# Kernel tuning notes

Measured on AMD Instinct MI355X. Metric: run time of the kernel, lower is better.

Reference implementation:

```python
import jax, jax.numpy as jnp
import numpy as np

D_MODEL = 1024
N_HEADS = 16
HEAD_DIM = D_MODEL // N_HEADS
B, T = 4, 2048
EPS = 1e-5


def _layernorm(x, w, b):
    mu = jnp.mean(x, axis=-1, keepdims=True)
    var = jnp.mean(jnp.square(x - mu), axis=-1, keepdims=True)
    return (x - mu) * jax.lax.rsqrt(var + EPS) * w + b


def _heads(x, w, b):
    # x: [B,T,D]; w stored [in,out] so y = x @ w + b (== torch Linear)
    y = x @ w + b
    return y.reshape(B, T, N_HEADS, HEAD_DIM).transpose(0, 2, 1, 3)  # [B,H,T,hd]


def _attention(q, k, v):
    scores = jnp.einsum('bhqd,bhkd->bhqk', q, k) / np.sqrt(HEAD_DIM).astype(np.float32)
    attn = jax.nn.softmax(scores, axis=-1)  # dropout is identity in eval mode
    o = jnp.einsum('bhqk,bhkd->bhqd', attn, v)
    return o.transpose(0, 2, 1, 3).reshape(B, T, D_MODEL)


def setup_inputs() -> dict:
    key = jax.random.key(0)
    ks = jax.random.split(key, 16)
    s = 1.0 / np.sqrt(D_MODEL)
    def lin(k, din, dout):
        kw, kb = jax.random.split(k)
        return (jax.random.uniform(kw, (din, dout), jnp.float32, -s, s),
                jax.random.uniform(kb, (dout,), jnp.float32, -s, s))
    inp = {}
    inp['temporal_tokens'] = jax.random.normal(ks[0], (B, T, D_MODEL), jnp.float32)
    inp['feature_tokens'] = jax.random.normal(ks[1], (B, T, D_MODEL), jnp.float32)
    names = ['qt', 'kf', 'vf', 'qf', 'kt', 'vt', 'ot', 'of']
    for i, n in enumerate(names):
        w, b = lin(ks[2 + i], D_MODEL, D_MODEL)
        inp[n + '_w'], inp[n + '_b'] = w, b
    inp['fus1_w'], inp['fus1_b'] = lin(ks[10], 2 * D_MODEL, D_MODEL)
    inp['fus2_w'], inp['fus2_b'] = lin(ks[11], D_MODEL, D_MODEL)
    for n in ['ln_fus', 'ln_t', 'ln_f']:
        inp[n + '_w'] = jnp.ones((D_MODEL,), jnp.float32)
        inp[n + '_b'] = jnp.zeros((D_MODEL,), jnp.float32)
    return inp


def reference(temporal_tokens, feature_tokens,
              qt_w, qt_b, kf_w, kf_b, vf_w, vf_b,
              qf_w, qf_b, kt_w, kt_b, vt_w, vt_b,
              ot_w, ot_b, of_w, of_b,
              fus1_w, fus1_b, fus2_w, fus2_b,
              ln_fus_w, ln_fus_b, ln_t_w, ln_t_b, ln_f_w, ln_f_b):
    # temporal -> feature cross attention
    Qt = _heads(temporal_tokens, qt_w, qt_b)
    Kf = _heads(feature_tokens, kf_w, kf_b)
    Vf = _heads(feature_tokens, vf_w, vf_b)
    attn_t = _attention(Qt, Kf, Vf) @ ot_w + ot_b
    fused_t = _layernorm(temporal_tokens + attn_t, ln_t_w, ln_t_b)
    # feature -> temporal cross attention
    Qf = _heads(feature_tokens, qf_w, qf_b)
    Kt = _heads(temporal_tokens, kt_w, kt_b)
    Vt = _heads(temporal_tokens, vt_w, vt_b)
    attn_f = _attention(Qf, Kt, Vt) @ of_w + of_b
    fused_f = _layernorm(feature_tokens + attn_f, ln_f_w, ln_f_b)
    # fusion MLP
    combined = jnp.concatenate([fused_t, fused_f], axis=-1)  # [B,T,2D]
    h = jax.nn.gelu(combined @ fus1_w + fus1_b, approximate=False)
    fused = _layernorm(h @ fus2_w + fus2_b, ln_fus_w, ln_fus_b)
    return fused
```

## Files before the change

### kernel.cpp

```cpp
#include <hip/hip_runtime.h>
#include <math.h>

typedef __attribute__((ext_vector_type(8))) short short8;
typedef __attribute__((ext_vector_type(4))) short short4v;
typedef __attribute__((ext_vector_type(4))) float floatx4;

#define GLOBAL_AS __attribute__((address_space(1)))
#define LDS_AS __attribute__((address_space(3)))

__device__ __forceinline__ float bf2f(unsigned short u) {
    unsigned int x = ((unsigned int)u) << 16;
    return __builtin_bit_cast(float, x);
}
__device__ __forceinline__ unsigned short f2bf(float f) {
    unsigned int u = __builtin_bit_cast(unsigned int, f);
    u += 0x7fffu + ((u >> 16) & 1u);
    return (unsigned short)(u >> 16);
}

__global__ __launch_bounds__(256) void cvt2_kernel(
    const float* __restrict__ a, const float* __restrict__ b,
    unsigned short* __restrict__ oa, unsigned short* __restrict__ ob)
{
    const int bx = blockIdx.x;
    const float* in = bx < 8192 ? a : b;
    unsigned short* out = bx < 8192 ? oa : ob;
    const size_t i = ((size_t)(bx & 8191) * 256 + threadIdx.x) * 4;
    float4 f = *(const float4*)(in + i);
    unsigned short o[4] = {f2bf(f.x), f2bf(f.y), f2bf(f.z), f2bf(f.w)};
    *(uint2*)(out + i) = *(const uint2*)o;
}

struct WX {
    const float* src[10];
    unsigned long long dst[10];
    int r64[10];
    int cum[11];
};

__global__ __launch_bounds__(256) void transpose_all_kernel(WX P, unsigned short* __restrict__ base)
{
    __shared__ unsigned short T[64][72];
    const int bx = blockIdx.x;
    int w = 0;
    #pragma unroll
    for (int i = 0; i < 10; ++i) if (bx >= P.cum[i + 1]) w = i + 1;
    const int tix = bx - P.cum[w];
    const int R = P.r64[w] * 64;
    const int r0 = (tix >> 4) * 64, c0 = (tix & 15) * 64;
    const float* in = P.src[w];
    unsigned short* out = base + P.dst[w];
    const int t = threadIdx.x;
    {
        const int r = t >> 2, cc = (t & 3) * 16;
        const float* p = in + (size_t)(r0 + r) * 1024 + c0 + cc;
        #pragma unroll
        for (int j = 0; j < 16; j += 4) {
            float4 f = *(const float4*)(p + j);
            T[cc + j + 0][r] = f2bf(f.x);
            T[cc + j + 1][r] = f2bf(f.y);
            T[cc + j + 2][r] = f2bf(f.z);
            T[cc + j + 3][r] = f2bf(f.w);
        }
    }
    __syncthreads();
    {
        const int c = t >> 2, rr = (t & 3) * 16;
        unsigned short* q = out + (size_t)(c0 + c) * R + r0 + rr;
        *(uint4*)(q)     = *(const uint4*)(&T[c][rr]);
        *(uint4*)(q + 8) = *(const uint4*)(&T[c][rr + 8]);
    }
}

__global__ __launch_bounds__(256) void head_transpose_kernel(
    const unsigned short* __restrict__ inA, unsigned short* __restrict__ outA,
    const unsigned short* __restrict__ inB, unsigned short* __restrict__ outB)
{
    __shared__ unsigned short T[64][72];
    const int z = blockIdx.z;
    const unsigned short* in = z < 4 ? inA : inB;
    unsigned short* out = z < 4 ? outA : outB;
    const int b = z & 3;
    const int t0 = blockIdx.x * 64;
    const int h = blockIdx.y;
    const int t = threadIdx.x;
    {
        const int r = t >> 2, cc = (t & 3) * 16;
        const unsigned short* p = in + (size_t)(b * 2048 + t0 + r) * 1024 + h * 64 + cc;
        unsigned short tmp[16];
        *(uint4*)(tmp)     = *(const uint4*)(p);
        *(uint4*)(tmp + 8) = *(const uint4*)(p + 8);
        #pragma unroll
        for (int j = 0; j < 16; ++j) T[cc + j][r] = tmp[j];
    }
    __syncthreads();
    {
        const int c = t >> 2, rr = (t & 3) * 16;
        unsigned short* q = out + ((size_t)(b * 16 + h) * 64 + c) * 2048 + t0 + rr;
        uint4 w0 = *(const uint4*)(&T[c][rr]);
        uint4 w1 = *(const uint4*)(&T[c][rr + 8]);
        if (c & 8) {
            w0 = (uint4){w0.z, w0.w, w0.x, w0.y};
            w1 = (uint4){w1.z, w1.w, w1.x, w1.y};
        }
        *(uint4*)(q)     = w0;
        *(uint4*)(q + 8) = w1;
    }
}

template <int MODE>
__global__ __launch_bounds__(256) void gemm_kernel(
    const unsigned short* __restrict__ A,
    const unsigned short* __restrict__ Wt,
    const float* __restrict__ bias,
    unsigned short* __restrict__ C,
    int M, int N, int K)
{
    __shared__ unsigned short As[128 * 32];
    __shared__ unsigned short Bs[128 * 32];
    const int bm = blockIdx.x * 128, bn = blockIdx.y * 128;
    const int tid = threadIdx.x;
    const int wave = tid >> 6, lane = tid & 63;
    const int quad = lane >> 4, l16 = lane & 15;
    const int wm = (wave & 1) * 64, wn = (wave >> 1) * 64;

    floatx4 acc[4][4];
    #pragma unroll
    for (int i = 0; i < 4; ++i)
        #pragma unroll
        for (int j = 0; j < 4; ++j) acc[i][j] = (floatx4){0.f, 0.f, 0.f, 0.f};

    const int srow = tid >> 2, scol = (tid & 3) * 8;
    const unsigned short* pa0 = A  + (size_t)(bm + srow) * K + scol;
    const unsigned short* pa1 = A  + (size_t)(bm + 64 + srow) * K + scol;
    const unsigned short* pb0 = Wt + (size_t)(bn + srow) * K + scol;
    const unsigned short* pb1 = Wt + (size_t)(bn + 64 + srow) * K + scol;
    unsigned short* la0 = As + wave * 512;
    unsigned short* la1 = As + 2048 + wave * 512;
    unsigned short* lb0 = Bs + wave * 512;
    unsigned short* lb1 = Bs + 2048 + wave * 512;

    int aoff[4], boff[4];
    #pragma unroll
    for (int i = 0; i < 4; ++i) {
        aoff[i] = (wm + i * 16 + l16) * 32 + quad * 8;
        boff[i] = (wn + i * 16 + l16) * 32 + quad * 8;
    }

    for (int k0 = 0; k0 < K; k0 += 32) {
        __builtin_amdgcn_global_load_lds((const GLOBAL_AS void*)(pa0 + k0), (LDS_AS void*)la0, 16, 0, 0);
        __builtin_amdgcn_global_load_lds((const GLOBAL_AS void*)(pa1 + k0), (LDS_AS void*)la1, 16, 0, 0);
        __builtin_amdgcn_global_load_lds((const GLOBAL_AS void*)(pb0 + k0), (LDS_AS void*)lb0, 16, 0, 0);
        __builtin_amdgcn_global_load_lds((const GLOBAL_AS void*)(pb1 + k0), (LDS_AS void*)lb1, 16, 0, 0);
        __syncthreads();
        short8 af[4], bf[4];
        #pragma unroll
        for (int i = 0; i < 4; ++i) {
            af[i] = *(const short8*)&As[aoff[i]];
            bf[i] = *(const short8*)&Bs[boff[i]];
        }
        #pragma unroll
        for (int mi = 0; mi < 4; ++mi)
            #pragma unroll
            for (int ni = 0; ni < 4; ++ni)
                acc[mi][ni] = __builtin_amdgcn_mfma_f32_16x16x32_bf16(
                    bf[ni], af[mi], acc[mi][ni], 0, 0, 0);
        __syncthreads();
    }

    float4 bv[4];
    #pragma unroll
    for (int ni = 0; ni < 4; ++ni)
        bv[ni] = *(const float4*)&bias[bn + wn + ni * 16 + quad * 4];
    #pragma unroll
    for (int mi = 0; mi < 4; ++mi) {
        const int m = bm + wm + mi * 16 + l16;
        #pragma unroll
        for (int ni = 0; ni < 4; ++ni) {
            const int n0 = bn + wn + ni * 16 + quad * 4;
            float v[4];
            #pragma unroll
            for (int r = 0; r < 4; ++r) v[r] = acc[mi][ni][r] + ((const float*)&bv[ni])[r];
            if (MODE == 2) {
                #pragma unroll
                for (int r = 0; r < 4; ++r)
                    v[r] = 0.5f * v[r] * (1.0f + erff(v[r] * 0.70710678118f));
            }
            unsigned short o[4] = {f2bf(v[0]), f2bf(v[1]), f2bf(v[2]), f2bf(v[3])};
            *(uint2*)&C[(size_t)m * N + n0] = *(const uint2*)o;
        }
    }
}

__global__ __launch_bounds__(256) void gemm_out_kernel(
    const unsigned short* __restrict__ A0, const unsigned short* __restrict__ W0,
    const float* __restrict__ bi0, const float* __restrict__ r0, unsigned short* __restrict__ C0,
    const unsigned short* __restrict__ A1, const unsigned short* __restrict__ W1,
    const float* __restrict__ bi1, const float* __restrict__ r1, unsigned short* __restrict__ C1)
{
    __shared__ unsigned short As[128 * 32];
    __shared__ unsigned short Bs[128 * 32];
    const int s = blockIdx.y >> 3;
    const unsigned short* A = s ? A1 : A0;
    const unsigned short* Wt = s ? W1 : W0;
    const float* bias = s ? bi1 : bi0;
    const float* resid = s ? r1 : r0;
    unsigned short* C = s ? C1 : C0;
    const int bm = blockIdx.x * 128, bn = (blockIdx.y & 7) * 128;
    const int tid = threadIdx.x;
    const int wave = tid >> 6, lane = tid & 63;
    const int quad = lane >> 4, l16 = lane & 15;
    const int wm = (wave & 1) * 64, wn = (wave >> 1) * 64;

    floatx4 acc[4][4];
    #pragma unroll
    for (int i = 0; i < 4; ++i)
        #pragma unroll
        for (int j = 0; j < 4; ++j) acc[i][j] = (floatx4){0.f, 0.f, 0.f, 0.f};

    const int srow = tid >> 2, scol = (tid & 3) * 8;
    const unsigned short* pa0 = A  + (size_t)(bm + srow) * 1024 + scol;
    const unsigned short* pa1 = A  + (size_t)(bm + 64 + srow) * 1024 + scol;
    const unsigned short* pb0 = Wt + (size_t)(bn + srow) * 1024 + scol;
    const unsigned short* pb1 = Wt + (size_t)(bn + 64 + srow) * 1024 + scol;
    unsigned short* la0 = As + wave * 512;
    unsigned short* la1 = As + 2048 + wave * 512;
    unsigned short* lb0 = Bs + wave * 512;
    unsigned short* lb1 = Bs + 2048 + wave * 512;

    int aoff[4], boff[4];
    #pragma unroll
    for (int i = 0; i < 4; ++i) {
        aoff[i] = (wm + i * 16 + l16) * 32 + quad * 8;
        boff[i] = (wn + i * 16 + l16) * 32 + quad * 8;
    }

    for (int k0 = 0; k0 < 1024; k0 += 32) {
        __builtin_amdgcn_global_load_lds((const GLOBAL_AS void*)(pa0 + k0), (LDS_AS void*)la0, 16, 0, 0);
        __builtin_amdgcn_global_load_lds((const GLOBAL_AS void*)(pa1 + k0), (LDS_AS void*)la1, 16, 0, 0);
        __builtin_amdgcn_global_load_lds((const GLOBAL_AS void*)(pb0 + k0), (LDS_AS void*)lb0, 16, 0, 0);
        __builtin_amdgcn_global_load_lds((const GLOBAL_AS void*)(pb1 + k0), (LDS_AS void*)lb1, 16, 0, 0);
        __syncthreads();
        short8 af[4], bf[4];
        #pragma unroll
        for (int i = 0; i < 4; ++i) {
            af[i] = *(const short8*)&As[aoff[i]];
            bf[i] = *(const short8*)&Bs[boff[i]];
        }
        #pragma unroll
        for (int mi = 0; mi < 4; ++mi)
            #pragma unroll
            for (int ni = 0; ni < 4; ++ni)
                acc[mi][ni] = __builtin_amdgcn_mfma_f32_16x16x32_bf16(
                    bf[ni], af[mi], acc[mi][ni], 0, 0, 0);
        __syncthreads();
    }

    float4 bv[4];
    #pragma unroll
    for (int ni = 0; ni < 4; ++ni)
        bv[ni] = *(const float4*)&bias[bn + wn + ni * 16 + quad * 4];
    #pragma unroll
    for (int mi = 0; mi < 4; ++mi) {
        const int m = bm + wm + mi * 16 + l16;
        #pragma unroll
        for (int ni = 0; ni < 4; ++ni) {
            const int n0 = bn + wn + ni * 16 + quad * 4;
            float4 rv = *(const float4*)&resid[(size_t)m * 1024 + n0];
            float v[4];
            v[0] = acc[mi][ni][0] + ((const float*)&bv[ni])[0] + rv.x;
            v[1] = acc[mi][ni][1] + ((const float*)&bv[ni])[1] + rv.y;
            v[2] = acc[mi][ni][2] + ((const float*)&bv[ni])[2] + rv.z;
            v[3] = acc[mi][ni][3] + ((const float*)&bv[ni])[3] + rv.w;
            unsigned short o[4] = {f2bf(v[0]), f2bf(v[1]), f2bf(v[2]), f2bf(v[3])};
            *(uint2*)&C[(size_t)m * 1024 + n0] = *(const uint2*)o;
        }
    }
}

__global__ __launch_bounds__(256) void gemm_qkv_kernel(
    const unsigned short* __restrict__ At, const unsigned short* __restrict__ Wt3t,
    const float* __restrict__ tb0, const float* __restrict__ tb1, const float* __restrict__ tb2,
    unsigned short* __restrict__ to0, unsigned short* __restrict__ to1, unsigned short* __restrict__ to2,
    const unsigned short* __restrict__ Af, const unsigned short* __restrict__ Wt3f,
    const float* __restrict__ fb0, const float* __restrict__ fb1, const float* __restrict__ fb2,
    unsigned short* __restrict__ fo0, unsigned short* __restrict__ fo1, unsigned short* __restrict__ fo2,
    float scale0)
{
    __shared__ unsigned short As[128 * 32];
    __shared__ unsigned short Bs[128 * 32];
    const int str = blockIdx.y >= 24;
    const unsigned short* A = str ? Af : At;
    const unsigned short* Wt = str ? Wt3f : Wt3t;
    const int byy = str ? (blockIdx.y - 24) : blockIdx.y;
    const int buf = byy >> 3;
    const int bn = byy * 128;
    const int cn = (byy & 7) * 128;
    const float* bias = str ? (buf == 0 ? fb0 : (buf == 1 ? fb1 : fb2))
                            : (buf == 0 ? tb0 : (buf == 1 ? tb1 : tb2));
    unsigned short* C = str ? (buf == 0 ? fo0 : (buf == 1 ? fo1 : fo2))
                            : (buf == 0 ? to0 : (buf == 1 ? to1 : to2));
    const float scale = buf == 0 ? scale0 : 1.0f;
    const int bm = blockIdx.x * 128;

    const int tid = threadIdx.x;
    const int wave = tid >> 6, lane = tid & 63;
    const int quad = lane >> 4, l16 = lane & 15;
    const int wm = (wave & 1) * 64, wn = (wave >> 1) * 64;

    floatx4 acc[4][4];
    #pragma unroll
    for (int i = 0; i < 4; ++i)
        #pragma unroll
        for (int j = 0; j < 4; ++j) acc[i][j] = (floatx4){0.f, 0.f, 0.f, 0.f};

    const int srow = tid >> 2, scol = (tid & 3) * 8;
    const unsigned short* pa0 = A  + (size_t)(bm + srow) * 1024 + scol;
    const unsigned short* pa1 = A  + (size_t)(bm + 64 + srow) * 1024 + scol;
    const unsigned short* pb0 = Wt + (size_t)(bn + srow) * 1024 + scol;
    const unsigned short* pb1 = Wt + (size_t)(bn + 64 + srow) * 1024 + scol;
    unsigned short* la0 = As + wave * 512;
    unsigned short* la1 = As + 2048 + wave * 512;
    unsigned short* lb0 = Bs + wave * 512;
    unsigned short* lb1 = Bs + 2048 + wave * 512;

    int aoff[4], boff[4];
    #pragma unroll
    for (int i = 0; i < 4; ++i) {
        aoff[i] = (wm + i * 16 + l16) * 32 + quad * 8;
        boff[i] = (wn + i * 16 + l16) * 32 + quad * 8;
    }

    for (int k0 = 0; k0 < 1024; k0 += 32) {
        __builtin_amdgcn_global_load_lds((const GLOBAL_AS void*)(pa0 + k0), (LDS_AS void*)la0, 16, 0, 0);
        __builtin_amdgcn_global_load_lds((const GLOBAL_AS void*)(pa1 + k0), (LDS_AS void*)la1, 16, 0, 0);
        __builtin_amdgcn_global_load_lds((const GLOBAL_AS void*)(pb0 + k0), (LDS_AS void*)lb0, 16, 0, 0);
        __builtin_amdgcn_global_load_lds((const GLOBAL_AS void*)(pb1 + k0), (LDS_AS void*)lb1, 16, 0, 0);
        __syncthreads();
        short8 af[4], bf[4];
        #pragma unroll
        for (int i = 0; i < 4; ++i) {
            af[i] = *(const short8*)&As[aoff[i]];
            bf[i] = *(const short8*)&Bs[boff[i]];
        }
        #pragma unroll
        for (int mi = 0; mi < 4; ++mi)
            #pragma unroll
            for (int ni = 0; ni < 4; ++ni)
                acc[mi][ni] = __builtin_amdgcn_mfma_f32_16x16x32_bf16(
                    bf[ni], af[mi], acc[mi][ni], 0, 0, 0);
        __syncthreads();
    }

    float4 bv[4];
    #pragma unroll
    for (int ni = 0; ni < 4; ++ni)
        bv[ni] = *(const float4*)&bias[cn + wn + ni * 16 + quad * 4];
    #pragma unroll
    for (int mi = 0; mi < 4; ++mi) {
        const int m = bm + wm + mi * 16 + l16;
        #pragma unroll
        for (int ni = 0; ni < 4; ++ni) {
            const int n0 = cn + wn + ni * 16 + quad * 4;
            unsigned short o[4];
            #pragma unroll
            for (int r = 0; r < 4; ++r)
                o[r] = f2bf((acc[mi][ni][r] + ((const float*)&bv[ni])[r]) * scale);
            *(uint2*)&C[(size_t)m * 1024 + n0] = *(const uint2*)o;
        }
    }
}

__global__ __launch_bounds__(256) void flash_kernel(
    const unsigned short* __restrict__ Q0, const unsigned short* __restrict__ K0,
    const unsigned short* __restrict__ V0, unsigned short* __restrict__ O0,
    const unsigned short* __restrict__ Q1, const unsigned short* __restrict__ K1,
    const unsigned short* __restrict__ V1, unsigned short* __restrict__ O1)
{
    __shared__ unsigned short Ks[64 * 64];
    __shared__ unsigned short Vs[64 * 64];

    const int z = blockIdx.z;
    const int s1 = z >= 4;
    const unsigned short* Q = s1 ? Q1 : Q0;
    const unsigned short* Kmat = s1 ? K1 : K0;
    const unsigned short* Vtp = s1 ? V1 : V0;
    unsigned short* O = s1 ? O1 : O0;
    const int b = z & 3;
    const int q0 = blockIdx.x * 128;
    const int h = blockIdx.y;
    const int tid = threadIdx.x;
    const int wave = tid >> 6, lane = tid & 63;
    const int quad = lane >> 4, l16 = lane & 15;

    const unsigned short* qp = Q + (size_t)(b * 2048 + q0 + wave * 32 + l16) * 1024 + h * 64;
    short8 qf[2][2];
    qf[0][0] = *(const short8*)(qp + quad * 8);
    qf[0][1] = *(const short8*)(qp + 32 + quad * 8);
    qf[1][0] = *(const short8*)(qp + 16 * 1024 + quad * 8);
    qf[1][1] = *(const short8*)(qp + 16 * 1024 + 32 + quad * 8);

    const int srow8 = lane >> 3;
    const int c8 = lane & 7;
    const int rit0 = wave * 16 + srow8;
    const int rit1 = rit0 + 8;
    const int col0 = (c8 ^ (rit0 & 7)) * 8;
    const int col1 = (c8 ^ (rit1 & 7)) * 8;
    const unsigned short* kbase = Kmat + (size_t)b * 2048 * 1024 + h * 64;
    const unsigned short* vbase = Vtp + (size_t)(b * 16 + h) * 64 * 2048;
    unsigned short* lk0 = Ks + (wave * 16) * 64;
    unsigned short* lk1 = lk0 + 8 * 64;
    unsigned short* lv0 = Vs + (wave * 16) * 64;
    unsigned short* lv1 = lv0 + 8 * 64;

    int koff[4][2];
    #pragma unroll
    for (int nt = 0; nt < 4; ++nt)
        #pragma unroll
        for (int hh = 0; hh < 2; ++hh)
            koff[nt][hh] = (nt * 16 + l16) * 64 + (((hh * 4 + quad) ^ (l16 & 7)) * 8);
    int voff[4][4];
    #pragma unroll
    for (int dt = 0; dt < 4; ++dt)
        #pragma unroll
        for (int nt = 0; nt < 4; ++nt)
            voff[dt][nt] = (dt * 16 + l16) * 64 +
                           (((nt * 2 + (quad >> 1)) ^ (l16 & 7)) * 8) +
                           (((quad & 1) ^ (l16 >> 3)) * 4);

    floatx4 oa[2][4], la[2];
    #pragma unroll
    for (int qg = 0; qg < 2; ++qg) {
        la[qg] = (floatx4){0.f, 0.f, 0.f, 0.f};
        #pragma unroll
        for (int dt = 0; dt < 4; ++dt) oa[qg][dt] = (floatx4){0.f, 0.f, 0.f, 0.f};
    }
    const short4v vone = {(short)0x3F80, (short)0x3F80, (short)0x3F80, (short)0x3F80};

    for (int kt = 0; kt < 32; ++kt) {
        const unsigned short* kg0 = kbase + (size_t)(kt * 64 + rit0) * 1024 + col0;
        const unsigned short* kg1 = kbase + (size_t)(kt * 64 + rit1) * 1024 + col1;
        const unsigned short* vg0 = vbase + (size_t)rit0 * 2048 + kt * 64 + col0;
        const unsigned short* vg1 = vbase + (size_t)rit1 * 2048 + kt * 64 + col1;
        __builtin_amdgcn_global_load_lds((const GLOBAL_AS void*)kg0, (LDS_AS void*)lk0, 16, 0, 0);
        __builtin_amdgcn_global_load_lds((const GLOBAL_AS void*)kg1, (LDS_AS void*)lk1, 16, 0, 0);
        __builtin_amdgcn_global_load_lds((const GLOBAL_AS void*)vg0, (LDS_AS void*)lv0, 16, 0, 0);
        __builtin_amdgcn_global_load_lds((const GLOBAL_AS void*)vg1, (LDS_AS void*)lv1, 16, 0, 0);
        __syncthreads();

        short4v pf[2][4];
        #pragma unroll
        for (int nt = 0; nt < 4; ++nt) {
            short8 k0 = *(const short8*)&Ks[koff[nt][0]];
            short8 k1 = *(const short8*)&Ks[koff[nt][1]];
            #pragma unroll
            for (int qg = 0; qg < 2; ++qg) {
                floatx4 s = (floatx4){0.f, 0.f, 0.f, 0.f};
                s = __builtin_amdgcn_mfma_f32_16x16x32_bf16(k0, qf[qg][0], s, 0, 0, 0);
                s = __builtin_amdgcn_mfma_f32_16x16x32_bf16(k1, qf[qg][1], s, 0, 0, 0);
                float p0 = __builtin_amdgcn_exp2f(s[0]);
                float p1 = __builtin_amdgcn_exp2f(s[1]);
                float p2 = __builtin_amdgcn_exp2f(s[2]);
                float p3 = __builtin_amdgcn_exp2f(s[3]);
                unsigned u0 = __builtin_bit_cast(unsigned, p0) + 0x8000u;
                unsigned u1 = __builtin_bit_cast(unsigned, p1) + 0x8000u;
                unsigned u2 = __builtin_bit_cast(unsigned, p2) + 0x8000u;
                unsigned u3 = __builtin_bit_cast(unsigned, p3) + 0x8000u;
                union { unsigned u[2]; short4v s4; } pk;
                pk.u[0] = __builtin_amdgcn_perm(u1, u0, 0x07060302u);
                pk.u[1] = __builtin_amdgcn_perm(u3, u2, 0x07060302u);
                pf[qg][nt] = pk.s4;
                la[qg] = __builtin_amdgcn_mfma_f32_16x16x16bf16_1k(vone, pf[qg][nt], la[qg], 0, 0, 0);
            }
        }
        #pragma unroll
        for (int dt = 0; dt < 4; ++dt)
            #pragma unroll
            for (int nt = 0; nt < 4; ++nt) {
                short4v vf = *(const short4v*)&Vs[voff[dt][nt]];
                oa[0][dt] = __builtin_amdgcn_mfma_f32_16x16x16bf16_1k(vf, pf[0][nt], oa[0][dt], 0, 0, 0);
                oa[1][dt] = __builtin_amdgcn_mfma_f32_16x16x16bf16_1k(vf, pf[1][nt], oa[1][dt], 0, 0, 0);
            }
        __syncthreads();
    }

    #pragma unroll
    for (int qg = 0; qg < 2; ++qg) {
        const float linv = 1.0f / la[qg][0];
        unsigned short* orow = O + (size_t)(b * 2048 + q0 + wave * 32 + qg * 16 + l16) * 1024 + h * 64;
        #pragma unroll
        for (int dt = 0; dt < 4; ++dt) {
            unsigned short ob[4];
            #pragma unroll
            for (int r = 0; r < 4; ++r) ob[r] = f2bf(oa[qg][dt][r] * linv);
            *(uint2*)(orow + dt * 16 + quad * 4) = *(const uint2*)ob;
        }
    }
}

__global__ __launch_bounds__(256) void ln2_kernel(
    const unsigned short* __restrict__ in0, const unsigned short* __restrict__ in1,
    unsigned short* __restrict__ out,
    const float* __restrict__ w0, const float* __restrict__ b0,
    const float* __restrict__ w1, const float* __restrict__ b1)
{
    __shared__ float red[8];
    const int sel = blockIdx.x >> 13;
    const int row = blockIdx.x & 8191;
    const unsigned short* in = sel ? in1 : in0;
    const float* w = sel ? w1 : w0;
    const float* bb = sel ? b1 : b0;
    const int tid = threadIdx.x;
    const int wave = tid >> 6, lane = tid & 63;
    uint2 raw = *(const uint2*)(in + (size_t)row * 1024 + tid * 4);
    float v[4];
    v[0] = bf2f((unsigned short)(raw.x & 0xffffu));
    v[1] = bf2f((unsigned short)(raw.x >> 16));
    v[2] = bf2f((unsigned short)(raw.y & 0xffffu));
    v[3] = bf2f((unsigned short)(raw.y >> 16));
    float s = v[0] + v[1] + v[2] + v[3];
    float sq = v[0] * v[0] + v[1] * v[1] + v[2] * v[2] + v[3] * v[3];
    #pragma unroll
    for (int m = 1; m < 64; m <<= 1) { s += __shfl_xor(s, m); sq += __shfl_xor(sq, m); }
    if (lane == 0) { red[wave] = s; red[4 + wave] = sq; }
    __syncthreads();
    s = red[0] + red[1] + red[2] + red[3];
    sq = red[4] + red[5] + red[6] + red[7];
    const float mu = s * (1.0f / 1024.0f);
    const float var = sq * (1.0f / 1024.0f) - mu * mu;
    const float rstd = rsqrtf(var + 1e-5f);
    unsigned short ob[4];
    #pragma unroll
    for (int j = 0; j < 4; ++j)
        ob[j] = f2bf((v[j] - mu) * rstd * w[tid * 4 + j] + bb[tid * 4 + j]);
    *(uint2*)(out + (size_t)row * 2048 + sel * 1024 + tid * 4) = *(uint2*)ob;
}

__global__ __launch_bounds__(256) void ln_final_kernel(
    const unsigned short* __restrict__ in, float* __restrict__ out,
    const float* __restrict__ w, const float* __restrict__ bias)
{
    __shared__ float red[8];
    const int row = blockIdx.x;
    const int tid = threadIdx.x;
    const int wave = tid >> 6, lane = tid & 63;
    uint2 raw = *(const uint2*)(in + (size_t)row * 1024 + tid * 4);
    float v[4];
    v[0] = bf2f((unsigned short)(raw.x & 0xffffu));
    v[1] = bf2f((unsigned short)(raw.x >> 16));
    v[2] = bf2f((unsigned short)(raw.y & 0xffffu));
    v[3] = bf2f((unsigned short)(raw.y >> 16));
    float s = v[0] + v[1] + v[2] + v[3];
    float sq = v[0] * v[0] + v[1] * v[1] + v[2] * v[2] + v[3] * v[3];
    #pragma unroll
    for (int m = 1; m < 64; m <<= 1) { s += __shfl_xor(s, m); sq += __shfl_xor(sq, m); }
    if (lane == 0) { red[wave] = s; red[4 + wave] = sq; }
    __syncthreads();
    s = red[0] + red[1] + red[2] + red[3];
    sq = red[4] + red[5] + red[6] + red[7];
    const float mu = s * (1.0f / 1024.0f);
    const float var = sq * (1.0f / 1024.0f) - mu * mu;
    const float rstd = rsqrtf(var + 1e-5f);
    float o[4];
    #pragma unroll
    for (int j = 0; j < 4; ++j)
        o[j] = (v[j] - mu) * rstd * w[tid * 4 + j] + bias[tid * 4 + j];
    *(float4*)(out + (size_t)row * 1024 + tid * 4) = (float4){o[0], o[1], o[2], o[3]};
}

extern "C" void kernel_launch(void* const* d_in, const int* in_sizes, int n_in,
                              void* d_out, int out_size, void* d_ws, size_t ws_size,
                              hipStream_t stream)
{
    (void)in_sizes; (void)n_in; (void)out_size; (void)ws_size;
    const float* temporal = (const float*)d_in[0];
    const float* feature  = (const float*)d_in[1];
    const float* qt_w = (const float*)d_in[2];
    const float* qt_b = (const float*)d_in[3];
    const float* kf_w = (const float*)d_in[4];
    const float* kf_b = (const float*)d_in[5];
    const float* vf_w = (const float*)d_in[6];
    const float* vf_b = (const float*)d_in[7];
    const float* qf_w = (const float*)d_in[8];
    const float* qf_b = (const float*)d_in[9];
    const float* kt_w = (const float*)d_in[10];
    const float* kt_b = (const float*)d_in[11];
    const float* vt_w = (const float*)d_in[12];
    const float* vt_b = (const float*)d_in[13];
    const float* ot_w = (const float*)d_in[14];
    const float* ot_b = (const float*)d_in[15];
    const float* of_w = (const float*)d_in[16];
    const float* of_b = (const float*)d_in[17];
    const float* fus1_w = (const float*)d_in[18];
    const float* fus1_b = (const float*)d_in[19];
    const float* fus2_w = (const float*)d_in[20];
    const float* fus2_b = (const float*)d_in[21];
    const float* ln_fus_w = (const float*)d_in[22];
    const float* ln_fus_b = (const float*)d_in[23];
    const float* ln_t_w = (const float*)d_in[24];
    const float* ln_t_b = (const float*)d_in[25];
    const float* ln_f_w = (const float*)d_in[26];
    const float* ln_f_b = (const float*)d_in[27];

    unsigned short* p = (unsigned short*)d_ws;
    const size_t EW = 1024ull * 1024;
    const size_t ET = 8192ull * 1024;
    unsigned short* WT3t = p;
    unsigned short* WT3f = p + 3 * EW;
    unsigned short* WTot = p + 6 * EW;
    unsigned short* WTof = p + 7 * EW;
    unsigned short* WTf1 = p + 8 * EW;
    unsigned short* WTf2 = p + 10 * EW;
    size_t off = 11 * EW;
    unsigned short* Tb = p + off; off += ET;
    unsigned short* Fb = p + off; off += ET;
    unsigned short* Qt = p + off; off += ET;
    unsigned short* Kt = p + off; off += ET;
    unsigned short* Vt = p + off; off += ET;
    unsigned short* Qf = p + off; off += ET;
    unsigned short* Kf = p + off; off += ET;
    unsigned short* Vf = p + off; off += ET;
    unsigned short* VfT = p + off; off += ET;
    unsigned short* VtT = p + off; off += ET;
    unsigned short* attnT = p + off; off += ET;
    unsigned short* attnF = p + off; off += ET;
    unsigned short* yT = Qt;
    unsigned short* yF = Qf;
    unsigned short* comb = Kt;
    unsigned short* hbuf = Kf;
    unsigned short* y2 = Vf;

    const float SC = 0.125f * 1.4426950408889634f;

    cvt2_kernel<<<16384, 256, 0, stream>>>(temporal, feature, Tb, Fb);

    {
        WX P;
        const float* srcs[10] = {qt_w, kt_w, vt_w, qf_w, kf_w, vf_w,
                                 ot_w, of_w, fus1_w, fus2_w};
        unsigned long long dsts[10] = {
            0, EW, 2 * EW,
            3 * EW, 4 * EW, 5 * EW,
            6 * EW, 7 * EW, 8 * EW, 10 * EW};
        int cum = 0;
        P.cum[0] = 0;
        for (int i = 0; i < 10; ++i) {
            P.src[i] = srcs[i];
            P.dst[i] = dsts[i];
            P.r64[i] = (i == 8) ? 32 : 16;
            cum += P.r64[i] * 16;
            P.cum[i + 1] = cum;
        }
        transpose_all_kernel<<<cum, 256, 0, stream>>>(P, p);
    }

    const dim3 gb(256);
    gemm_qkv_kernel<<<dim3(64, 48), gb, 0, stream>>>(
        Tb, WT3t, qt_b, kt_b, vt_b, Qt, Kt, Vt,
        Fb, WT3f, qf_b, kf_b, vf_b, Qf, Kf, Vf, SC);
    head_transpose_kernel<<<dim3(32, 16, 8), gb, 0, stream>>>(Vf, VfT, Vt, VtT);
    flash_kernel<<<dim3(16, 16, 8), gb, 0, stream>>>(
        Qt, Kf, VfT, attnT, Qf, Kt, VtT, attnF);
    gemm_out_kernel<<<dim3(64, 16), gb, 0, stream>>>(
        attnT, WTot, ot_b, temporal, yT,
        attnF, WTof, of_b, feature,  yF);
    ln2_kernel<<<16384, gb, 0, stream>>>(yT, yF, comb, ln_t_w, ln_t_b, ln_f_w, ln_f_b);
    gemm_kernel<2><<<dim3(64, 8), gb, 0, stream>>>(comb, WTf1, fus1_b, hbuf, 8192, 1024, 2048);
    gemm_kernel<0><<<dim3(64, 8), gb, 0, stream>>>(hbuf, WTf2, fus2_b, y2, 8192, 1024, 1024);
    ln_final_kernel<<<8192, gb, 0, stream>>>(y2, (float*)d_out, ln_fus_w, ln_fus_b);
}
```

Measured before the change: 717.2 us.

## Double GEMM K-tile with XOR-swizzled LDS and fuse V head-transpose into QKV epilogue

All three GEMM kernels now share a macro core that stages a K=64 tile per iteration instead of 32, which halves the number of barrier pairs per K sweep. The LDS layout is XOR-swizzled by row to avoid bank conflicts on the fragment reads. The QKV GEMM epilogue writes the V projection directly in the transposed, swizzled per-head layout the flash kernel expects, which removes the separate head_transpose kernel and its extra round trip through memory. In exchange, LDS use per block doubles, and the V stores become scalar 2-byte strided writes that may coalesce poorly.

```diff
diff --git a/kernel.cpp b/kernel.cpp
--- a/kernel.cpp
+++ b/kernel.cpp
@@ -72,41 +72,60 @@
     }
 }
 
-__global__ __launch_bounds__(256) void head_transpose_kernel(
-    const unsigned short* __restrict__ inA, unsigned short* __restrict__ outA,
-    const unsigned short* __restrict__ inB, unsigned short* __restrict__ outB)
-{
-    __shared__ unsigned short T[64][72];
-    const int z = blockIdx.z;
-    const unsigned short* in = z < 4 ? inA : inB;
-    unsigned short* out = z < 4 ? outA : outB;
-    const int b = z & 3;
-    const int t0 = blockIdx.x * 64;
-    const int h = blockIdx.y;
-    const int t = threadIdx.x;
-    {
-        const int r = t >> 2, cc = (t & 3) * 16;
-        const unsigned short* p = in + (size_t)(b * 2048 + t0 + r) * 1024 + h * 64 + cc;
-        unsigned short tmp[16];
-        *(uint4*)(tmp)     = *(const uint4*)(p);
-        *(uint4*)(tmp + 8) = *(const uint4*)(p + 8);
-        #pragma unroll
-        for (int j = 0; j < 16; ++j) T[cc + j][r] = tmp[j];
-    }
-    __syncthreads();
-    {
-        const int c = t >> 2, rr = (t & 3) * 16;
-        unsigned short* q = out + ((size_t)(b * 16 + h) * 64 + c) * 2048 + t0 + rr;
-        uint4 w0 = *(const uint4*)(&T[c][rr]);
-        uint4 w1 = *(const uint4*)(&T[c][rr + 8]);
-        if (c & 8) {
-            w0 = (uint4){w0.z, w0.w, w0.x, w0.y};
-            w1 = (uint4){w1.z, w1.w, w1.x, w1.y};
-        }
-        *(uint4*)(q)     = w0;
-        *(uint4*)(q + 8) = w1;
-    }
-}
+#define GEMM_CORE(A_, B_, Kdim)                                               \
+    const int tid = threadIdx.x;                                              \
+    const int wave = tid >> 6, lane = tid & 63;                               \
+    const int quad = lane >> 4, l16 = lane & 15;                              \
+    const int wm = (wave & 1) * 64, wn = (wave >> 1) * 64;                    \
+    const int srow8 = lane >> 3, c8 = lane & 7;                               \
+    const int scol = (c8 ^ srow8) * 8;                                        \
+    floatx4 acc[4][4];                                                        \
+    _Pragma("unroll")                                                         \
+    for (int i = 0; i < 4; ++i)                                               \
+        _Pragma("unroll")                                                     \
+        for (int j = 0; j < 4; ++j) acc[i][j] = (floatx4){0.f, 0.f, 0.f, 0.f};\
+    const unsigned short* pa[4];                                              \
+    const unsigned short* pb[4];                                              \
+    _Pragma("unroll")                                                         \
+    for (int i = 0; i < 4; ++i) {                                             \
+        pa[i] = (A_) + (size_t)(bm + i * 32 + wave * 8 + srow8) * (Kdim) + scol; \
+        pb[i] = (B_) + (size_t)(bn + i * 32 + wave * 8 + srow8) * (Kdim) + scol; \
+    }                                                                         \
+    int aoff[4][2], boff[4][2];                                               \
+    _Pragma("unroll")                                                         \
+    for (int i = 0; i < 4; ++i)                                               \
+        _Pragma("unroll")                                                     \
+        for (int s = 0; s < 2; ++s) {                                         \
+            const int cg = ((s * 4 + quad) ^ (l16 & 7)) * 8;                  \
+            aoff[i][s] = (wm + i * 16 + l16) * 64 + cg;                       \
+            boff[i][s] = (wn + i * 16 + l16) * 64 + cg;                       \
+        }                                                                     \
+    for (int k0 = 0; k0 < (Kdim); k0 += 64) {                                 \
+        _Pragma("unroll")                                                     \
+        for (int i = 0; i < 4; ++i) {                                         \
+            __builtin_amdgcn_global_load_lds((const GLOBAL_AS void*)(pa[i] + k0), \
+                (LDS_AS void*)(As + i * 2048 + wave * 512), 16, 0, 0);        \
+            __builtin_amdgcn_global_load_lds((const GLOBAL_AS void*)(pb[i] + k0), \
+                (LDS_AS void*)(Bs + i * 2048 + wave * 512), 16, 0, 0);        \
+        }                                                                     \
+        __syncthreads();                                                      \
+        _Pragma("unroll")                                                     \
+        for (int s = 0; s < 2; ++s) {                                         \
+            short8 af[4], bf[4];                                              \
+            _Pragma("unroll")                                                 \
+            for (int i = 0; i < 4; ++i) {                                     \
+                af[i] = *(const short8*)&As[aoff[i][s]];                      \
+                bf[i] = *(const short8*)&Bs[boff[i][s]];                      \
+            }                                                                 \
+            _Pragma("unroll")                                                 \
+            for (int mi = 0; mi < 4; ++mi)                                    \
+                _Pragma("unroll")                                             \
+                for (int ni = 0; ni < 4; ++ni)                                \
+                    acc[mi][ni] = __builtin_amdgcn_mfma_f32_16x16x32_bf16(    \
+                        bf[ni], af[mi], acc[mi][ni], 0, 0, 0);                \
+        }                                                                     \
+        __syncthreads();                                                      \
+    }
 
 template <int MODE>
 __global__ __launch_bounds__(256) void gemm_kernel(
@@ -114,59 +133,12 @@
     const unsigned short* __restrict__ Wt,
     const float* __restrict__ bias,
     unsigned short* __restrict__ C,
-    int M, int N, int K)
-{
-    __shared__ unsigned short As[128 * 32];
-    __shared__ unsigned short Bs[128 * 32];
+    int N, int K)
+{
+    __shared__ unsigned short As[128 * 64];
+    __shared__ unsigned short Bs[128 * 64];
     const int bm = blockIdx.x * 128, bn = blockIdx.y * 128;
-    const int tid = threadIdx.x;
-    const int wave = tid >> 6, lane = tid & 63;
-    const int quad = lane >> 4, l16 = lane & 15;
-    const int wm = (wave & 1) * 64, wn = (wave >> 1) * 64;
-
-    floatx4 acc[4][4];
-    #pragma unroll
-    for (int i = 0; i < 4; ++i)
-        #pragma unroll
-        for (int j = 0; j < 4; ++j) acc[i][j] = (floatx4){0.f, 0.f, 0.f, 0.f};
-
-    const int srow = tid >> 2, scol = (tid & 3) * 8;
-    const unsigned short* pa0 = A  + (size_t)(bm + srow) * K + scol;
-    const unsigned short* pa1 = A  + (size_t)(bm + 64 + srow) * K + scol;
-    const unsigned short* pb0 = Wt + (size_t)(bn + srow) * K + scol;
-    const unsigned short* pb1 = Wt + (size_t)(bn + 64 + srow) * K + scol;
-    unsigned short* la0 = As + wave * 512;
-    unsigned short* la1 = As + 2048 + wave * 512;
-    unsigned short* lb0 = Bs + wave * 512;
-    unsigned short* lb1 = Bs + 2048 + wave * 512;
-
-    int aoff[4], boff[4];
-    #pragma unroll
-    for (int i = 0; i < 4; ++i) {
-        aoff[i] = (wm + i * 16 + l16) * 32 + quad * 8;
-        boff[i] = (wn + i * 16 + l16) * 32 + quad * 8;
-    }
-
-    for (int k0 = 0; k0 < K; k0 += 32) {
-        __builtin_amdgcn_global_load_lds((const GLOBAL_AS void*)(pa0 + k0), (LDS_AS void*)la0, 16, 0, 0);
-        __builtin_amdgcn_global_load_lds((const GLOBAL_AS void*)(pa1 + k0), (LDS_AS void*)la1, 16, 0, 0);
-        __builtin_amdgcn_global_load_lds((const GLOBAL_AS void*)(pb0 + k0), (LDS_AS void*)lb0, 16, 0, 0);
-        __builtin_amdgcn_global_load_lds((const GLOBAL_AS void*)(pb1 + k0), (LDS_AS void*)lb1, 16, 0, 0);
-        __syncthreads();
-        short8 af[4], bf[4];
-        #pragma unroll
-        for (int i = 0; i < 4; ++i) {
-            af[i] = *(const short8*)&As[aoff[i]];
-            bf[i] = *(const short8*)&Bs[boff[i]];
-        }
-        #pragma unroll
-        for (int mi = 0; mi < 4; ++mi)
-            #pragma unroll
-            for (int ni = 0; ni < 4; ++ni)
-                acc[mi][ni] = __builtin_amdgcn_mfma_f32_16x16x32_bf16(
-                    bf[ni], af[mi], acc[mi][ni], 0, 0, 0);
-        __syncthreads();
-    }
+    GEMM_CORE(A, Wt, K)
 
     float4 bv[4];
     #pragma unroll
@@ -198,63 +170,16 @@
     const unsigned short* __restrict__ A1, const unsigned short* __restrict__ W1,
     const float* __restrict__ bi1, const float* __restrict__ r1, unsigned short* __restrict__ C1)
 {
-    __shared__ unsigned short As[128 * 32];
-    __shared__ unsigned short Bs[128 * 32];
-    const int s = blockIdx.y >> 3;
-    const unsigned short* A = s ? A1 : A0;
-    const unsigned short* Wt = s ? W1 : W0;
-    const float* bias = s ? bi1 : bi0;
-    const float* resid = s ? r1 : r0;
-    unsigned short* C = s ? C1 : C0;
+    __shared__ unsigned short As[128 * 64];
+    __shared__ unsigned short Bs[128 * 64];
+    const int s1 = blockIdx.y >> 3;
+    const unsigned short* A = s1 ? A1 : A0;
+    const unsigned short* Wt = s1 ? W1 : W0;
+    const float* bias = s1 ? bi1 : bi0;
+    const float* resid = s1 ? r1 : r0;
+    unsigned short* C = s1 ? C1 : C0;
     const int bm = blockIdx.x * 128, bn = (blockIdx.y & 7) * 128;
-    const int tid = threadIdx.x;
-    const int wave = tid >> 6, lane = tid & 63;
-    const int quad = lane >> 4, l16 = lane & 15;
-    const int wm = (wave & 1) * 64, wn = (wave >> 1) * 64;
-
-    floatx4 acc[4][4];
-    #pragma unroll
-    for (int i = 0; i < 4; ++i)
-        #pragma unroll
-        for (int j = 0; j < 4; ++j) acc[i][j] = (floatx4){0.f, 0.f, 0.f, 0.f};
-
-    const int srow = tid >> 2, scol = (tid & 3) * 8;
-    const unsigned short* pa0 = A  + (size_t)(bm + srow) * 1024 + scol;
-    const unsigned short* pa1 = A  + (size_t)(bm + 64 + srow) * 1024 + scol;
-    const unsigned short* pb0 = Wt + (size_t)(bn + srow) * 1024 + scol;
-    const unsigned short* pb1 = Wt + (size_t)(bn + 64 + srow) * 1024 + scol;
-    unsigned short* la0 = As + wave * 512;
-    unsigned short* la1 = As + 2048 + wave * 512;
-    unsigned short* lb0 = Bs + wave * 512;
-    unsigned short* lb1 = Bs + 2048 + wave * 512;
-
-    int aoff[4], boff[4];
-    #pragma unroll
-    for (int i = 0; i < 4; ++i) {
-        aoff[i] = (wm + i * 16 + l16) * 32 + quad * 8;
-        boff[i] = (wn + i * 16 + l16) * 32 + quad * 8;
-    }
-
-    for (int k0 = 0; k0 < 1024; k0 += 32) {
-        __builtin_amdgcn_global_load_lds((const GLOBAL_AS void*)(pa0 + k0), (LDS_AS void*)la0, 16, 0, 0);
-        __builtin_amdgcn_global_load_lds((const GLOBAL_AS void*)(pa1 + k0), (LDS_AS void*)la1, 16, 0, 0);
-        __builtin_amdgcn_global_load_lds((const GLOBAL_AS void*)(pb0 + k0), (LDS_AS void*)lb0, 16, 0, 0);
-        __builtin_amdgcn_global_load_lds((const GLOBAL_AS void*)(pb1 + k0), (LDS_AS void*)lb1, 16, 0, 0);
-        __syncthreads();
-        short8 af[4], bf[4];
-        #pragma unroll
-        for (int i = 0; i < 4; ++i) {
-            af[i] = *(const short8*)&As[aoff[i]];
-            bf[i] = *(const short8*)&Bs[boff[i]];
-        }
-        #pragma unroll
-        for (int mi = 0; mi < 4; ++mi)
-            #pragma unroll
-            for (int ni = 0; ni < 4; ++ni)
-                acc[mi][ni] = __builtin_amdgcn_mfma_f32_16x16x32_bf16(
-                    bf[ni], af[mi], acc[mi][ni], 0, 0, 0);
-        __syncthreads();
-    }
+    GEMM_CORE(A, Wt, 1024)
 
     float4 bv[4];
     #pragma unroll
@@ -287,8 +212,8 @@
     unsigned short* __restrict__ fo0, unsigned short* __restrict__ fo1, unsigned short* __restrict__ fo2,
     float scale0)
 {
-    __shared__ unsigned short As[128 * 32];
-    __shared__ unsigned short Bs[128 * 32];
+    __shared__ unsigned short As[128 * 64];
+    __shared__ unsigned short Bs[128 * 64];
     const int str = blockIdx.y >= 24;
     const unsigned short* A = str ? Af : At;
     const unsigned short* Wt = str ? Wt3f : Wt3t;
@@ -302,55 +227,7 @@
                             : (buf == 0 ? to0 : (buf == 1 ? to1 : to2));
     const float scale = buf == 0 ? scale0 : 1.0f;
     const int bm = blockIdx.x * 128;
-
-    const int tid = threadIdx.x;
-    const int wave = tid >> 6, lane = tid & 63;
-    const int quad = lane >> 4, l16 = lane & 15;
-    const int wm = (wave & 1) * 64, wn = (wave >> 1) * 64;
-
-    floatx4 acc[4][4];
-    #pragma unroll
-    for (int i = 0; i < 4; ++i)
-        #pragma unroll
-        for (int j = 0; j < 4; ++j) acc[i][j] = (floatx4){0.f, 0.f, 0.f, 0.f};
-
-    const int srow = tid >> 2, scol = (tid & 3) * 8;
-    const unsigned short* pa0 = A  + (size_t)(bm + srow) * 1024 + scol;
-    const unsigned short* pa1 = A  + (size_t)(bm + 64 + srow) * 1024 + scol;
-    const unsigned short* pb0 = Wt + (size_t)(bn + srow) * 1024 + scol;
-    const unsigned short* pb1 = Wt + (size_t)(bn + 64 + srow) * 1024 + scol;
-    unsigned short* la0 = As + wave * 512;
-    unsigned short* la1 = As + 2048 + wave * 512;
-    unsigned short* lb0 = Bs + wave * 512;
-    unsigned short* lb1 = Bs + 2048 + wave * 512;
-
-    int aoff[4], boff[4];
-    #pragma unroll
-    for (int i = 0; i < 4; ++i) {
-        aoff[i] = (wm + i * 16 + l16) * 32 + quad * 8;
-        boff[i] = (wn + i * 16 + l16) * 32 + quad * 8;
-    }
-
-    for (int k0 = 0; k0 < 1024; k0 += 32) {
-        __builtin_amdgcn_global_load_lds((const GLOBAL_AS void*)(pa0 + k0), (LDS_AS void*)la0, 16, 0, 0);
-        __builtin_amdgcn_global_load_lds((const GLOBAL_AS void*)(pa1 + k0), (LDS_AS void*)la1, 16, 0, 0);
-        __builtin_amdgcn_global_load_lds((const GLOBAL_AS void*)(pb0 + k0), (LDS_AS void*)lb0, 16, 0, 0);
-        __builtin_amdgcn_global_load_lds((const GLOBAL_AS void*)(pb1 + k0), (LDS_AS void*)lb1, 16, 0, 0);
-        __syncthreads();
-        short8 af[4], bf[4];
-        #pragma unroll
-        for (int i = 0; i < 4; ++i) {
-            af[i] = *(const short8*)&As[aoff[i]];
-            bf[i] = *(const short8*)&Bs[boff[i]];
-        }
-        #pragma unroll
-        for (int mi = 0; mi < 4; ++mi)
-            #pragma unroll
-            for (int ni = 0; ni < 4; ++ni)
-                acc[mi][ni] = __builtin_amdgcn_mfma_f32_16x16x32_bf16(
-                    bf[ni], af[mi], acc[mi][ni], 0, 0, 0);
-        __syncthreads();
-    }
+    GEMM_CORE(A, Wt, 1024)
 
     float4 bv[4];
     #pragma unroll
@@ -366,7 +243,16 @@
             #pragma unroll
             for (int r = 0; r < 4; ++r)
                 o[r] = f2bf((acc[mi][ni][r] + ((const float*)&bv[ni])[r]) * scale);
-            *(uint2*)&C[(size_t)m * 1024 + n0] = *(const uint2*)o;
+            if (buf == 2) {
+                const int b = m >> 11, t = m & 2047;
+                const int h = n0 >> 6, d0 = n0 & 63;
+                const int tsw = t ^ ((d0 & 8) ? 4 : 0);
+                unsigned short* vb = C + ((size_t)(b * 16 + h) * 64) * 2048 + tsw;
+                #pragma unroll
+                for (int r = 0; r < 4; ++r) vb[(size_t)(d0 + r) * 2048] = o[r];
+            } else {
+                *(uint2*)&C[(size_t)m * 1024 + n0] = *(const uint2*)o;
+            }
         }
     }
 }
@@ -629,6 +515,7 @@
     unsigned short* comb = Kt;
     unsigned short* hbuf = Kf;
     unsigned short* y2 = Vf;
+    (void)Vt;
 
     const float SC = 0.125f * 1.4426950408889634f;
 
@@ -656,16 +543,15 @@
 
     const dim3 gb(256);
     gemm_qkv_kernel<<<dim3(64, 48), gb, 0, stream>>>(
-        Tb, WT3t, qt_b, kt_b, vt_b, Qt, Kt, Vt,
-        Fb, WT3f, qf_b, kf_b, vf_b, Qf, Kf, Vf, SC);
-    head_transpose_kernel<<<dim3(32, 16, 8), gb, 0, stream>>>(Vf, VfT, Vt, VtT);
+        Tb, WT3t, qt_b, kt_b, vt_b, Qt, Kt, VtT,
+        Fb, WT3f, qf_b, kf_b, vf_b, Qf, Kf, VfT, SC);
     flash_kernel<<<dim3(16, 16, 8), gb, 0, stream>>>(
         Qt, Kf, VfT, attnT, Qf, Kt, VtT, attnF);
     gemm_out_kernel<<<dim3(64, 16), gb, 0, stream>>>(
         attnT, WTot, ot_b, temporal, yT,
         attnF, WTof, of_b, feature,  yF);
     ln2_kernel<<<16384, gb, 0, stream>>>(yT, yF, comb, ln_t_w, ln_t_b, ln_f_w, ln_f_b);
-    gemm_kernel<2><<<dim3(64, 8), gb, 0, stream>>>(comb, WTf1, fus1_b, hbuf, 8192, 1024, 2048);
-    gemm_kernel<0><<<dim3(64, 8), gb, 0, stream>>>(hbuf, WTf2, fus2_b, y2, 8192, 1024, 1024);
+    gemm_kernel<2><<<dim3(64, 8), gb, 0, stream>>>(comb, WTf1, fus1_b, hbuf, 1024, 2048);
+    gemm_kernel<0><<<dim3(64, 8), gb, 0, stream>>>(hbuf, WTf2, fus2_b, y2, 1024, 1024);
     ln_final_kernel<<<8192, gb, 0, stream>>>(y2, (float*)d_out, ln_fus_w, ln_fus_b);
 }
```

Result: faster. 673.8 us (-6.1%).
